# Optimization experiments

Measured on AMD Instinct MI355X. Metric: run time of the kernel, lower is better.

## Reference

```python
import jax, jax.numpy as jnp
import numpy as np

EMBED = 1024
HEAD = 64
SEQ = 2048
BATCH = 8


def setup_inputs() -> dict:
    key = jax.random.key(0)
    kx, kq, kk, kv = jax.random.split(key, 4)
    x = jax.random.normal(kx, (BATCH, SEQ, EMBED), dtype=jnp.float32)
    # torch nn.Linear weight is [out,in]; we store [in,out] so y = x @ W
    Wq = jax.random.normal(kq, (EMBED, HEAD), dtype=jnp.float32) * (EMBED ** -0.5)
    Wk = jax.random.normal(kk, (EMBED, HEAD), dtype=jnp.float32) * (EMBED ** -0.5)
    Wv = jax.random.normal(kv, (EMBED, HEAD), dtype=jnp.float32) * (EMBED ** -0.5)
    return {"x": x, "Wq": Wq, "Wk": Wk, "Wv": Wv}


def reference(x, Wq, Wk, Wv):
    # x: [B,T,C]; single-head causal attention. Scale uses C (embedding dim),
    # matching the original module's C ** (-0.5). Dropout in eval mode (identity).
    B, T, C = x.shape
    q = x @ Wq  # [B,T,H]
    k = x @ Wk  # [B,T,H]
    v = x @ Wv  # [B,T,H]
    scores = jnp.einsum('bqh,bkh->bqk', q, k) * (C ** -0.5)  # [B,T,T]
    causal = jnp.tril(jnp.ones((T, T), dtype=bool))
    scores = jnp.where(causal, scores, -jnp.inf)
    weights = jax.nn.softmax(scores, axis=-1)
    return jnp.einsum('bqk,bkh->bqh', weights, v)  # [B,T,H]
```

## Files before the change

### kernel.cpp

```cpp
#include <hip/hip_runtime.h>
#include <hip/hip_bf16.h>
#include <math.h>

#define BATCH 8
#define SEQ 2048
#define EMBED 1024
#define HEAD 64
#define NROWS (BATCH*SEQ)

typedef short bf16x8 __attribute__((ext_vector_type(8)));
typedef short bf16x4 __attribute__((ext_vector_type(4)));
typedef float f32x4  __attribute__((ext_vector_type(4)));

__device__ inline short f2bf(float f) {
    __hip_bfloat16 h = __float2bfloat16(f);
    return *(short*)&h;
}
__device__ inline float bf2f(short s) {
    __hip_bfloat16 h = *(__hip_bfloat16*)&s;
    return __bfloat162float(h);
}

__device__ __host__ inline int triOff(int qt) {
    int g = qt >> 3;
    return 4 * g * (g + 1) + (qt & 7) * (g + 1);
}
#define NSLOT 80

__global__ __launch_bounds__(256) void prep_w(
    const float* __restrict__ Wq, const float* __restrict__ Wk,
    const float* __restrict__ Wv, short* __restrict__ wt)
{
    int g    = blockIdx.x * 256 + threadIdx.x;
    int lane = g & 63;
    int frag = g >> 6;
    int k32  = frag & 31;
    int ct   = frag >> 5;
    int col  = ct * 16 + (lane & 15);
    int mm   = col >> 6, cc = col & 63;
    const float* W = (mm == 0) ? Wq : ((mm == 1) ? Wk : Wv);
    int kb = k32 * 32 + (lane >> 4) * 8;
    bf16x8 o;
#pragma unroll
    for (int j = 0; j < 8; j++)
        o[j] = f2bf(W[(size_t)(kb + j) * HEAD + cc]);
    *(bf16x8*)&wt[(size_t)g * 8] = o;
}

#define XS_STRIDE 152
__global__ __launch_bounds__(256) void proj_kernel(
    const float* __restrict__ x, const short* __restrict__ wt,
    short* __restrict__ q, short* __restrict__ k, short* __restrict__ v)
{
    __shared__ short xs[32][XS_STRIDE];

    const int tid  = threadIdx.x;
    const int wave = tid >> 6, lane = tid & 63;
    const int m16  = lane & 15, quad = lane >> 4;
    const int r0   = blockIdx.x * 32;

    f32x4 acc[2][3];
#pragma unroll
    for (int i = 0; i < 2; i++)
#pragma unroll
        for (int j = 0; j < 3; j++) acc[i][j] = (f32x4){0.f, 0.f, 0.f, 0.f};

    const int srow = tid >> 5;
    const int skf  = tid & 31;

    for (int c = 0; c < 8; c++) {
        const int k0 = c * 128;
        float4 xv[4];
#pragma unroll
        for (int i = 0; i < 4; i++)
            xv[i] = *(const float4*)&x[(size_t)(r0 + srow + i * 8) * EMBED + k0 + skf * 4];
        __syncthreads();
#pragma unroll
        for (int i = 0; i < 4; i++) {
            bf16x4 xb;
            xb[0] = f2bf(xv[i].x); xb[1] = f2bf(xv[i].y);
            xb[2] = f2bf(xv[i].z); xb[3] = f2bf(xv[i].w);
            *(bf16x4*)&xs[srow + i * 8][skf * 4] = xb;
        }
        __syncthreads();

#pragma unroll
        for (int s = 0; s < 4; s++) {
            bf16x8 a0 = *(const bf16x8*)&xs[m16][s * 32 + quad * 8];
            bf16x8 a1 = *(const bf16x8*)&xs[16 + m16][s * 32 + quad * 8];
            int k32 = c * 4 + s;
#pragma unroll
            for (int j = 0; j < 3; j++) {
                int ct = wave * 3 + j;
                bf16x8 bb = *(const bf16x8*)&wt[(size_t)((ct * 32 + k32) * 64 + lane) * 8];
                acc[0][j] = __builtin_amdgcn_mfma_f32_16x16x32_bf16(a0, bb, acc[0][j], 0, 0, 0);
                acc[1][j] = __builtin_amdgcn_mfma_f32_16x16x32_bf16(a1, bb, acc[1][j], 0, 0, 0);
            }
        }
    }

#pragma unroll
    for (int i = 0; i < 2; i++) {
#pragma unroll
        for (int j = 0; j < 3; j++) {
            int gcol = wave * 48 + j * 16 + m16;
            int mm = gcol >> 6, cc = gcol & 63;
            short* op = (mm == 0) ? q : ((mm == 1) ? k : v);
#pragma unroll
            for (int reg = 0; reg < 4; reg++) {
                int row = r0 + i * 16 + quad * 4 + reg;
                op[(size_t)row * HEAD + cc] = f2bf(acc[i][j][reg]);
            }
        }
    }
}

__global__ __launch_bounds__(256) void attn_kernel(
    const short* __restrict__ qg, const short* __restrict__ kg,
    const short* __restrict__ vg,
    short* __restrict__ pO, float* __restrict__ pl)
{
    __shared__ short ksh[64][88];
    __shared__ short vsh[64][88];
    __shared__ short psh[4][16][88];

    const int qt  = blockIdx.x;
    const int seg = blockIdx.y;
    const int b   = blockIdx.z;
    const int c0  = seg * 8;
    const int c1  = min(seg * 8 + 8, qt + 1);
    if (c0 >= c1) return;

    const int tid  = threadIdx.x;
    const int wave = tid >> 6, lane = tid & 63;
    const int m16  = lane & 15, quad = lane >> 4;
    const float scale = 0.03125f;

    const short* qb = qg + (size_t)b * SEQ * HEAD;
    const short* kb = kg + (size_t)b * SEQ * HEAD;
    const short* vb = vg + (size_t)b * SEQ * HEAD;

    bf16x8 a_q[2];
    {
        const int qrow = qt * 64 + wave * 16 + m16;
        a_q[0] = *(const bf16x8*)&qb[(size_t)qrow * HEAD + quad * 8];
        a_q[1] = *(const bf16x8*)&qb[(size_t)qrow * HEAD + 32 + quad * 8];
    }

    f32x4 o_acc[4];
#pragma unroll
    for (int i = 0; i < 4; i++) o_acc[i] = (f32x4){0.f, 0.f, 0.f, 0.f};
    float lsum[4] = {0.f, 0.f, 0.f, 0.f};

    const int krow = tid >> 3;
    const int ks8  = tid & 7;
    const int vp0  = tid >> 3;
    const int vh0  = (tid & 7) * 8;
    const int vpp  = vp0 ^ ((tid & 7) << 2);

    for (int c = c0; c < c1; c++) {
        const int t0 = c * 64;
        __syncthreads();
        {
            bf16x8 k0v = *(const bf16x8*)&kb[(size_t)(t0 + krow) * HEAD + ks8 * 8];
            bf16x8 k1v = *(const bf16x8*)&kb[(size_t)(t0 + 32 + krow) * HEAD + ks8 * 8];
            *(bf16x8*)&ksh[krow][ks8 * 8]      = k0v;
            *(bf16x8*)&ksh[32 + krow][ks8 * 8] = k1v;
        }
        {
            bf16x8 v0 = *(const bf16x8*)&vb[(size_t)(t0 + 2 * vp0) * HEAD + vh0];
            bf16x8 v1 = *(const bf16x8*)&vb[(size_t)(t0 + 2 * vp0 + 1) * HEAD + vh0];
#pragma unroll
            for (int j = 0; j < 8; j++) {
                int hh = vh0 + j;
                int val = (v0[j] & 0xffff) | (((int)v1[j]) << 16);
                *(int*)&vsh[hh][vpp * 2] = val;
            }
        }
        __syncthreads();

        f32x4 s_t[4];
#pragma unroll
        for (int nt = 0; nt < 4; nt++) {
            bf16x8 bk0 = *(const bf16x8*)&ksh[nt * 16 + m16][quad * 8];
            bf16x8 bk1 = *(const bf16x8*)&ksh[nt * 16 + m16][32 + quad * 8];
            f32x4 acc = (f32x4){0.f, 0.f, 0.f, 0.f};
            acc = __builtin_amdgcn_mfma_f32_16x16x32_bf16(a_q[0], bk0, acc, 0, 0, 0);
            acc = __builtin_amdgcn_mfma_f32_16x16x32_bf16(a_q[1], bk1, acc, 0, 0, 0);
            s_t[nt] = acc;
        }

#pragma unroll
        for (int r = 0; r < 4; r++) {
            const int row = qt * 64 + wave * 16 + quad * 4 + r;
#pragma unroll
            for (int nt = 0; nt < 4; nt++) {
                int t = t0 + nt * 16 + m16;
                float p = (t <= row) ? __expf(s_t[nt][r] * scale) : 0.f;
                lsum[r] += p;
                psh[wave][quad * 4 + r][nt * 16 + m16] = f2bf(p);
            }
        }

#pragma unroll
        for (int s = 0; s < 2; s++) {
            bf16x8 a_p = *(const bf16x8*)&psh[wave][m16][s * 32 + quad * 8];
#pragma unroll
            for (int ht = 0; ht < 4; ht++) {
                int hh = ht * 16 + m16;
                int pb = (s * 16 + quad * 4) ^ (((hh >> 3) & 7) << 2);
                bf16x8 b_v = *(const bf16x8*)&vsh[hh][pb * 2];
                o_acc[ht] = __builtin_amdgcn_mfma_f32_16x16x32_bf16(a_p, b_v, o_acc[ht], 0, 0, 0);
            }
        }
    }

#pragma unroll
    for (int r = 0; r < 4; r++) {
#pragma unroll
        for (int off = 8; off >= 1; off >>= 1)
            lsum[r] += __shfl_xor(lsum[r], off, 64);
    }
    const size_t slot  = (size_t)b * NSLOT + triOff(qt) + seg;
    const size_t pbase = slot * 64;
#pragma unroll
    for (int ht = 0; ht < 4; ht++) {
#pragma unroll
        for (int r = 0; r < 4; r++) {
            int rowt = wave * 16 + quad * 4 + r;
            pO[(pbase + rowt) * 64 + ht * 16 + m16] = f2bf(o_acc[ht][r]);
        }
    }
    if (m16 == 0) {
#pragma unroll
        for (int r = 0; r < 4; r++) {
            int rowt = wave * 16 + quad * 4 + r;
            pl[pbase + rowt] = lsum[r];
        }
    }
}

__global__ __launch_bounds__(256) void combine_kernel(
    const short* __restrict__ pO, const float* __restrict__ pl,
    float* __restrict__ out)
{
    int g   = blockIdx.x * 256 + threadIdx.x;
    int h   = g & 63;
    int row = (g >> 6) & 2047;
    int b   = g >> 17;
    int qt  = row >> 6, lr = row & 63;
    int ns  = (qt >> 3) + 1;
    size_t base = (size_t)b * NSLOT + triOff(qt);
    float O = 0.f, L = 0.f;
    for (int s = 0; s < ns; s++) {
        O += bf2f(pO[((base + s) * 64 + lr) * 64 + h]);
        L += pl[(base + s) * 64 + lr];
    }
    out[g] = O / L;
}

extern "C" void kernel_launch(void* const* d_in, const int* in_sizes, int n_in,
                              void* d_out, int out_size, void* d_ws, size_t ws_size,
                              hipStream_t stream) {
    const float* x  = (const float*)d_in[0];
    const float* Wq = (const float*)d_in[1];
    const float* Wk = (const float*)d_in[2];
    const float* Wv = (const float*)d_in[3];
    float* out = (float*)d_out;

    short* q  = (short*)d_ws;
    short* k  = q + (size_t)NROWS * HEAD;
    short* v  = k + (size_t)NROWS * HEAD;
    short* wt = v + (size_t)NROWS * HEAD;
    short* pO = wt + 196608;
    float* pl = (float*)(pO + (size_t)BATCH * NSLOT * 64 * 64);

    prep_w<<<96, 256, 0, stream>>>(Wq, Wk, Wv, wt);
    proj_kernel<<<512, 256, 0, stream>>>(x, wt, q, k, v);
    attn_kernel<<<dim3(32, 4, 8), 256, 0, stream>>>(q, k, v, pO, pl);
    combine_kernel<<<4096, 256, 0, stream>>>(pO, pl, out);
}
```

Baseline: 144.7 us.

## Halve tile sizes, prefetch loads, split attention finer, vectorize combine

The projection kernel now handles 16 rows per block instead of 32, with a register prefetch of the next x chunk, and twice as many blocks are launched. The attention kernel splits the KV range into segments of 4 tiles instead of 8, which doubles the number of slots. It also prefetches the next K/V tile into registers and skips the causal mask on tiles that are not on the diagonal. The combine kernel reads 4 head elements per thread with vector loads and multiplies by a reciprocal. The aim is more parallelism and latency hiding for the 256 CUs, at the cost of more partial outputs to combine and less reuse of the weights in the projection.

```diff
diff --git a/kernel.cpp b/kernel.cpp
--- a/kernel.cpp
+++ b/kernel.cpp
@@ -21,11 +21,11 @@
     return __bfloat162float(h);
 }
 
+#define NSLOT 144
 __device__ __host__ inline int triOff(int qt) {
-    int g = qt >> 3;
-    return 4 * g * (g + 1) + (qt & 7) * (g + 1);
-}
-#define NSLOT 80
+    int g = qt >> 2;
+    return 2 * g * (g + 1) + (qt & 3) * (g + 1);
+}
 
 __global__ __launch_bounds__(256) void prep_w(
     const float* __restrict__ Wq, const float* __restrict__ Wk,
@@ -52,65 +52,62 @@
     const float* __restrict__ x, const short* __restrict__ wt,
     short* __restrict__ q, short* __restrict__ k, short* __restrict__ v)
 {
-    __shared__ short xs[32][XS_STRIDE];
+    __shared__ short xs[16][XS_STRIDE];
 
     const int tid  = threadIdx.x;
     const int wave = tid >> 6, lane = tid & 63;
     const int m16  = lane & 15, quad = lane >> 4;
-    const int r0   = blockIdx.x * 32;
-
-    f32x4 acc[2][3];
-#pragma unroll
-    for (int i = 0; i < 2; i++)
-#pragma unroll
-        for (int j = 0; j < 3; j++) acc[i][j] = (f32x4){0.f, 0.f, 0.f, 0.f};
-
-    const int srow = tid >> 5;
-    const int skf  = tid & 31;
+    const int r0   = blockIdx.x * 16;
+
+    f32x4 acc[3];
+#pragma unroll
+    for (int j = 0; j < 3; j++) acc[j] = (f32x4){0.f, 0.f, 0.f, 0.f};
+
+    const int srow = tid >> 4;
+    const int skf  = tid & 15;
+
+    const float* xrow = x + (size_t)(r0 + srow) * EMBED;
+    float4 xv0 = *(const float4*)&xrow[skf * 4];
+    float4 xv1 = *(const float4*)&xrow[64 + skf * 4];
 
     for (int c = 0; c < 8; c++) {
-        const int k0 = c * 128;
-        float4 xv[4];
-#pragma unroll
-        for (int i = 0; i < 4; i++)
-            xv[i] = *(const float4*)&x[(size_t)(r0 + srow + i * 8) * EMBED + k0 + skf * 4];
         __syncthreads();
-#pragma unroll
-        for (int i = 0; i < 4; i++) {
-            bf16x4 xb;
-            xb[0] = f2bf(xv[i].x); xb[1] = f2bf(xv[i].y);
-            xb[2] = f2bf(xv[i].z); xb[3] = f2bf(xv[i].w);
-            *(bf16x4*)&xs[srow + i * 8][skf * 4] = xb;
+        {
+            bf16x4 b0, b1;
+            b0[0] = f2bf(xv0.x); b0[1] = f2bf(xv0.y);
+            b0[2] = f2bf(xv0.z); b0[3] = f2bf(xv0.w);
+            b1[0] = f2bf(xv1.x); b1[1] = f2bf(xv1.y);
+            b1[2] = f2bf(xv1.z); b1[3] = f2bf(xv1.w);
+            *(bf16x4*)&xs[srow][skf * 4]      = b0;
+            *(bf16x4*)&xs[srow][64 + skf * 4] = b1;
         }
         __syncthreads();
-
+        if (c < 7) {
+            xv0 = *(const float4*)&xrow[(c + 1) * 128 + skf * 4];
+            xv1 = *(const float4*)&xrow[(c + 1) * 128 + 64 + skf * 4];
+        }
 #pragma unroll
         for (int s = 0; s < 4; s++) {
             bf16x8 a0 = *(const bf16x8*)&xs[m16][s * 32 + quad * 8];
-            bf16x8 a1 = *(const bf16x8*)&xs[16 + m16][s * 32 + quad * 8];
             int k32 = c * 4 + s;
 #pragma unroll
             for (int j = 0; j < 3; j++) {
                 int ct = wave * 3 + j;
                 bf16x8 bb = *(const bf16x8*)&wt[(size_t)((ct * 32 + k32) * 64 + lane) * 8];
-                acc[0][j] = __builtin_amdgcn_mfma_f32_16x16x32_bf16(a0, bb, acc[0][j], 0, 0, 0);
-                acc[1][j] = __builtin_amdgcn_mfma_f32_16x16x32_bf16(a1, bb, acc[1][j], 0, 0, 0);
-            }
-        }
-    }
-
-#pragma unroll
-    for (int i = 0; i < 2; i++) {
-#pragma unroll
-        for (int j = 0; j < 3; j++) {
-            int gcol = wave * 48 + j * 16 + m16;
-            int mm = gcol >> 6, cc = gcol & 63;
-            short* op = (mm == 0) ? q : ((mm == 1) ? k : v);
-#pragma unroll
-            for (int reg = 0; reg < 4; reg++) {
-                int row = r0 + i * 16 + quad * 4 + reg;
-                op[(size_t)row * HEAD + cc] = f2bf(acc[i][j][reg]);
-            }
+                acc[j] = __builtin_amdgcn_mfma_f32_16x16x32_bf16(a0, bb, acc[j], 0, 0, 0);
+            }
+        }
+    }
+
+#pragma unroll
+    for (int j = 0; j < 3; j++) {
+        int gcol = wave * 48 + j * 16 + m16;
+        int mm = gcol >> 6, cc = gcol & 63;
+        short* op = (mm == 0) ? q : ((mm == 1) ? k : v);
+#pragma unroll
+        for (int reg = 0; reg < 4; reg++) {
+            int row = r0 + quad * 4 + reg;
+            op[(size_t)row * HEAD + cc] = f2bf(acc[j][reg]);
         }
     }
 }
@@ -127,8 +124,8 @@
     const int qt  = blockIdx.x;
     const int seg = blockIdx.y;
     const int b   = blockIdx.z;
-    const int c0  = seg * 8;
-    const int c1  = min(seg * 8 + 8, qt + 1);
+    const int c0  = seg * 4;
+    const int c1  = min(seg * 4 + 4, qt + 1);
     if (c0 >= c1) return;
 
     const int tid  = threadIdx.x;
@@ -158,26 +155,32 @@
     const int vh0  = (tid & 7) * 8;
     const int vpp  = vp0 ^ ((tid & 7) << 2);
 
+    bf16x8 kr0 = *(const bf16x8*)&kb[(size_t)(c0 * 64 + krow) * HEAD + ks8 * 8];
+    bf16x8 kr1 = *(const bf16x8*)&kb[(size_t)(c0 * 64 + 32 + krow) * HEAD + ks8 * 8];
+    bf16x8 vr0 = *(const bf16x8*)&vb[(size_t)(c0 * 64 + 2 * vp0) * HEAD + vh0];
+    bf16x8 vr1 = *(const bf16x8*)&vb[(size_t)(c0 * 64 + 2 * vp0 + 1) * HEAD + vh0];
+
     for (int c = c0; c < c1; c++) {
         const int t0 = c * 64;
         __syncthreads();
         {
-            bf16x8 k0v = *(const bf16x8*)&kb[(size_t)(t0 + krow) * HEAD + ks8 * 8];
-            bf16x8 k1v = *(const bf16x8*)&kb[(size_t)(t0 + 32 + krow) * HEAD + ks8 * 8];
-            *(bf16x8*)&ksh[krow][ks8 * 8]      = k0v;
-            *(bf16x8*)&ksh[32 + krow][ks8 * 8] = k1v;
-        }
-        {
-            bf16x8 v0 = *(const bf16x8*)&vb[(size_t)(t0 + 2 * vp0) * HEAD + vh0];
-            bf16x8 v1 = *(const bf16x8*)&vb[(size_t)(t0 + 2 * vp0 + 1) * HEAD + vh0];
+            *(bf16x8*)&ksh[krow][ks8 * 8]      = kr0;
+            *(bf16x8*)&ksh[32 + krow][ks8 * 8] = kr1;
 #pragma unroll
             for (int j = 0; j < 8; j++) {
                 int hh = vh0 + j;
-                int val = (v0[j] & 0xffff) | (((int)v1[j]) << 16);
+                int val = (vr0[j] & 0xffff) | (((int)vr1[j]) << 16);
                 *(int*)&vsh[hh][vpp * 2] = val;
             }
         }
         __syncthreads();
+        if (c + 1 < c1) {
+            const int tn = (c + 1) * 64;
+            kr0 = *(const bf16x8*)&kb[(size_t)(tn + krow) * HEAD + ks8 * 8];
+            kr1 = *(const bf16x8*)&kb[(size_t)(tn + 32 + krow) * HEAD + ks8 * 8];
+            vr0 = *(const bf16x8*)&vb[(size_t)(tn + 2 * vp0) * HEAD + vh0];
+            vr1 = *(const bf16x8*)&vb[(size_t)(tn + 2 * vp0 + 1) * HEAD + vh0];
+        }
 
         f32x4 s_t[4];
 #pragma unroll
@@ -190,15 +193,27 @@
             s_t[nt] = acc;
         }
 
-#pragma unroll
-        for (int r = 0; r < 4; r++) {
-            const int row = qt * 64 + wave * 16 + quad * 4 + r;
-#pragma unroll
-            for (int nt = 0; nt < 4; nt++) {
-                int t = t0 + nt * 16 + m16;
-                float p = (t <= row) ? __expf(s_t[nt][r] * scale) : 0.f;
-                lsum[r] += p;
-                psh[wave][quad * 4 + r][nt * 16 + m16] = f2bf(p);
+        if (c == qt) {
+#pragma unroll
+            for (int r = 0; r < 4; r++) {
+                const int row = qt * 64 + wave * 16 + quad * 4 + r;
+#pragma unroll
+                for (int nt = 0; nt < 4; nt++) {
+                    int t = t0 + nt * 16 + m16;
+                    float p = (t <= row) ? __expf(s_t[nt][r] * scale) : 0.f;
+                    lsum[r] += p;
+                    psh[wave][quad * 4 + r][nt * 16 + m16] = f2bf(p);
+                }
+            }
+        } else {
+#pragma unroll
+            for (int r = 0; r < 4; r++) {
+#pragma unroll
+                for (int nt = 0; nt < 4; nt++) {
+                    float p = __expf(s_t[nt][r] * scale);
+                    lsum[r] += p;
+                    psh[wave][quad * 4 + r][nt * 16 + m16] = f2bf(p);
+                }
             }
         }
 
@@ -245,18 +260,23 @@
     float* __restrict__ out)
 {
     int g   = blockIdx.x * 256 + threadIdx.x;
-    int h   = g & 63;
-    int row = (g >> 6) & 2047;
-    int b   = g >> 17;
+    int h4  = (g & 15) * 4;
+    int row = (g >> 4) & 2047;
+    int b   = g >> 15;
     int qt  = row >> 6, lr = row & 63;
-    int ns  = (qt >> 3) + 1;
+    int ns  = (qt >> 2) + 1;
     size_t base = (size_t)b * NSLOT + triOff(qt);
-    float O = 0.f, L = 0.f;
+    float4 O = {0.f, 0.f, 0.f, 0.f};
+    float  L = 0.f;
     for (int s = 0; s < ns; s++) {
-        O += bf2f(pO[((base + s) * 64 + lr) * 64 + h]);
+        bf16x4 ov = *(const bf16x4*)&pO[((base + s) * 64 + lr) * 64 + h4];
+        O.x += bf2f(ov[0]); O.y += bf2f(ov[1]);
+        O.z += bf2f(ov[2]); O.w += bf2f(ov[3]);
         L += pl[(base + s) * 64 + lr];
     }
-    out[g] = O / L;
+    float inv = 1.f / L;
+    O.x *= inv; O.y *= inv; O.z *= inv; O.w *= inv;
+    *(float4*)&out[(size_t)g * 4] = O;
 }
 
 extern "C" void kernel_launch(void* const* d_in, const int* in_sizes, int n_in,
@@ -276,7 +296,7 @@
     float* pl = (float*)(pO + (size_t)BATCH * NSLOT * 64 * 64);
 
     prep_w<<<96, 256, 0, stream>>>(Wq, Wk, Wv, wt);
-    proj_kernel<<<512, 256, 0, stream>>>(x, wt, q, k, v);
-    attn_kernel<<<dim3(32, 4, 8), 256, 0, stream>>>(q, k, v, pO, pl);
-    combine_kernel<<<4096, 256, 0, stream>>>(pO, pl, out);
-}
+    proj_kernel<<<1024, 256, 0, stream>>>(x, wt, q, k, v);
+    attn_kernel<<<dim3(32, 8, 8), 256, 0, stream>>>(q, k, v, pO, pl);
+    combine_kernel<<<1024, 256, 0, stream>>>(pO, pl, out);
+}
```

Result: faster. 138.2 us (-4.4%).
